# Optimization experiments

Hardware: AMD Instinct MI355X
Metric: run time of the kernel (lower is better)

## Reference

```python
import jax, jax.numpy as jnp
import numpy as np

B, C, H, W, D = 2, 256, 40, 40, 40
HEADS = 8


def _conv1x1(x, w, b):
    # 1x1x1 Conv3d == pointwise channel mix: x [B,C,H,W,D], w [O,C], b [O]
    return jnp.einsum('bchwd,oc->bohwd', x, w) + b[None, :, None, None, None]


def setup_inputs() -> dict:
    key = jax.random.key(0)
    ks = jax.random.split(key, 9)
    s = 1.0 / np.sqrt(C)
    return {
        'x': jax.random.normal(ks[0], (B, C, H, W, D), dtype=jnp.float32),
        'wq': jax.random.normal(ks[1], (C, C), dtype=jnp.float32) * s,
        'bq': jax.random.normal(ks[2], (C,), dtype=jnp.float32) * 0.01,
        'wk': jax.random.normal(ks[3], (C, C), dtype=jnp.float32) * s,
        'bk': jax.random.normal(ks[4], (C,), dtype=jnp.float32) * 0.01,
        'wv': jax.random.normal(ks[5], (C, C), dtype=jnp.float32) * s,
        'bv': jax.random.normal(ks[6], (C,), dtype=jnp.float32) * 0.01,
        'wp': jax.random.normal(ks[7], (C, C), dtype=jnp.float32) * s,
        'bp': jax.random.normal(ks[8], (C,), dtype=jnp.float32) * 0.01,
    }


def reference(x, wq, bq, wk, bk, wv, bv, wp, bp):
    b, ch, h, w, d = x.shape
    heads = HEADS
    hd = ch // heads
    scale = hd ** -0.5
    # q/k/v projections are identical across the three branches -> compute once
    q = _conv1x1(x, wq, bq)
    k = _conv1x1(x, wk, bk)
    v = _conv1x1(x, wv, bv)

    def branch(s1, s2, s3):
        # row-major reshape, exactly matching torch .view semantics
        qh = q.reshape(b, heads, hd, s1, s2, s3)
        kh = k.reshape(b, heads, hd, s1, s2, s3)
        vh = v.reshape(b, heads, hd, s1, s2, s3)
        # matmul over last two axes: attend along s2 with s3 as feature dim
        attn = jax.nn.softmax(qh @ jnp.swapaxes(kh, -1, -2) * scale, axis=-1)
        return (attn @ vh).reshape(b, ch, h, w, d)

    out = branch(h, w, d) + branch(w, h, d) + branch(d, h, w)
    return _conv1x1(out, wp, bp)
```

## Files before the change

### kernel.cpp

```cpp
#include <hip/hip_runtime.h>

#define NB 2
#define NC 256
#define NHH 40
#define NSP 64000
#define PL 1600
#define SCALE 0.17677669529663687f

typedef unsigned short u16;
typedef unsigned int   u32;

typedef __attribute__((ext_vector_type(8))) short bf16x8;
typedef __attribute__((ext_vector_type(4))) float f32x4;

__device__ __forceinline__ float bf2f(u16 u) {
    union { u32 i; float f; } c; c.i = ((u32)u) << 16; return c.f;
}
__device__ __forceinline__ u16 f2bf(float f) {
    union { u32 i; float f; } c; c.f = f; u32 x = c.i;
    return (u16)((x + 0x7fffu + ((x >> 16) & 1u)) >> 16);
}
__device__ __forceinline__ u32 pack2(float a, float b) {
    return (u32)f2bf(a) | ((u32)f2bf(b) << 16);
}
__device__ __forceinline__ f32x4 zero4() {
    f32x4 z; z[0] = 0.f; z[1] = 0.f; z[2] = 0.f; z[3] = 0.f; return z;
}
__device__ __forceinline__ bf16x8 zero8() {
    bf16x8 z;
#pragma unroll
    for (int e = 0; e < 8; ++e) z[e] = 0;
    return z;
}

__global__ __launch_bounds__(256) void wcvt3(
    const float* __restrict__ wq, const float* __restrict__ wk,
    const float* __restrict__ wv, u16* __restrict__ dst)
{
    const int g   = blockIdx.x * 256 + threadIdx.x;
    const int mat = g >> 14;
    const int off = (g & 16383) << 2;
    const float* s = (mat == 0) ? wq : ((mat == 1) ? wk : wv);
    const float4 f = *(const float4*)(s + off);
    ushort4 p;
    p.x = f2bf(f.x); p.y = f2bf(f.y); p.z = f2bf(f.z); p.w = f2bf(f.w);
    *(ushort4*)(dst + (mat << 16) + off) = p;
}

__global__ __launch_bounds__(256) void wcvt1(
    const float* __restrict__ w, u16* __restrict__ dst)
{
    const int g   = blockIdx.x * 256 + threadIdx.x;
    const int off = g << 2;
    const float4 f = *(const float4*)(w + off);
    ushort4 p;
    p.x = f2bf(f.x); p.y = f2bf(f.y); p.z = f2bf(f.z); p.w = f2bf(f.w);
    *(ushort4*)(dst + off) = p;
}

__global__ __launch_bounds__(256, 2) void qkv_mfma(
    const float* __restrict__ x, const u16* __restrict__ wb,
    const float* __restrict__ bq, const float* __restrict__ bk,
    const float* __restrict__ bv,
    u16* __restrict__ q, u16* __restrict__ k, u16* __restrict__ v)
{
    const int b    = blockIdx.z;
    const int n0   = blockIdx.x * 64;
    const int t    = threadIdx.x;
    const int lane = t & 63;
    const int wid  = t >> 6;
    const int o0w  = wid * 64;

    __shared__ u16 xs[64][264];
    __shared__ u16 wsm[2][256][40];

    const float* xb = x + (size_t)b * NC * NSP;

    {
        const int p   = t >> 4;
        const int nn  = (t & 15) << 2;
        const int rot = (t >> 1) & 3;
#pragma unroll
        for (int it = 0; it < 8; ++it) {
            const int c = (it * 16 + p) * 2;
            const float4 fa = *(const float4*)(xb + (size_t)c * NSP + n0 + nn);
            const float4 fb = *(const float4*)(xb + (size_t)(c + 1) * NSP + n0 + nn);
            u32 pk[4] = { pack2(fa.x, fb.x), pack2(fa.y, fb.y),
                          pack2(fa.z, fb.z), pack2(fa.w, fb.w) };
#pragma unroll
            for (int kk = 0; kk < 4; ++kk) {
                const int k2 = (kk + rot) & 3;
                *(u32*)&xs[nn + k2][c] = pk[k2];
            }
        }
    }

    {
        const u16* ws0 = wb + t * NC;
#pragma unroll
        for (int mm = 0; mm < 4; ++mm)
            *(bf16x8*)&wsm[0][t][mm * 8] = *(const bf16x8*)(ws0 + mm * 8);
    }
    __syncthreads();

    f32x4 acc[4][4];
#pragma unroll
    for (int i = 0; i < 4; ++i)
#pragma unroll
        for (int j = 0; j < 4; ++j) acc[i][j] = zero4();

    const int row = lane & 15;
    const int kg  = (lane >> 4) << 3;

    int cur = 0;
    for (int step = 0; step < 24; ++step) {
        const int m  = step >> 3;
        const int kc = step & 7;
        const bool pf = (step + 1 < 24);

        bf16x8 wreg[4];
        if (pf) {
            const int m2  = (step + 1) >> 3;
            const int kc2 = (step + 1) & 7;
            const u16* ws2 = wb + (m2 << 16) + t * NC + kc2 * 32;
#pragma unroll
            for (int mm = 0; mm < 4; ++mm)
                wreg[mm] = *(const bf16x8*)(ws2 + mm * 8);
        }

        bf16x8 af[4], bfr[4];
#pragma unroll
        for (int i = 0; i < 4; ++i)
            af[i] = *(const bf16x8*)&wsm[cur][o0w + 16 * i + row][kg];
#pragma unroll
        for (int j = 0; j < 4; ++j)
            bfr[j] = *(const bf16x8*)&xs[16 * j + row][kc * 32 + kg];
#pragma unroll
        for (int i = 0; i < 4; ++i)
#pragma unroll
            for (int j = 0; j < 4; ++j)
                acc[i][j] = __builtin_amdgcn_mfma_f32_16x16x32_bf16(
                    af[i], bfr[j], acc[i][j], 0, 0, 0);

        if (pf) {
#pragma unroll
            for (int mm = 0; mm < 4; ++mm)
                *(bf16x8*)&wsm[cur ^ 1][t][mm * 8] = wreg[mm];
        }

        if (kc == 7) {
            u16* op = ((m == 0) ? q : ((m == 1) ? k : v)) + (size_t)b * NC * NSP;
            const float* bm = (m == 0) ? bq : ((m == 1) ? bk : bv);
#pragma unroll
            for (int i = 0; i < 4; ++i) {
#pragma unroll
                for (int r = 0; r < 4; ++r) {
                    const int o = o0w + 16 * i + ((lane >> 4) << 2) + r;
                    const float bb = bm[o];
#pragma unroll
                    for (int j = 0; j < 4; ++j) {
                        const int n = n0 + 16 * j + row;
                        op[(size_t)o * NSP + n] = f2bf(acc[i][j][r] + bb);
                    }
                }
            }
#pragma unroll
            for (int i = 0; i < 4; ++i)
#pragma unroll
                for (int j = 0; j < 4; ++j) acc[i][j] = zero4();
        }

        if (pf) {
            __syncthreads();
            cur ^= 1;
        }
    }
}

__global__ __launch_bounds__(64, 4) void attn_mfma(
    const u16* __restrict__ q, const u16* __restrict__ k,
    const u16* __restrict__ v, u16* __restrict__ a)
{
    const int s = blockIdx.x;
    const size_t base = (size_t)s * PL;
    const int l = threadIdx.x & 63;
    const int g = l >> 4;
    const int c = l & 15;

    __shared__ u16 vs[48][56];
    __shared__ u16 ps[48][56];

#pragma unroll
    for (int it = 0; it < 3; ++it) {
        const int t = l + it * 64;
        *(u32*)&vs[t >> 2][40 + ((t & 3) << 1)] = 0u;
    }

#pragma unroll
    for (int it = 0; it < 7; ++it) {
        const int idx = l + it * 64;
        if (idx < 400) {
            const int j = idx / 10, d4 = (idx % 10) << 2;
            const ushort4 vv = *(const ushort4*)(v + base + j * 40 + d4);
            vs[d4 + 0][j] = vv.x; vs[d4 + 1][j] = vv.y;
            vs[d4 + 2][j] = vv.z; vs[d4 + 3][j] = vv.w;
        }
    }

    f32x4 sacc[3][3];
#pragma unroll
    for (int mt = 0; mt < 3; ++mt)
#pragma unroll
        for (int jt = 0; jt < 3; ++jt) sacc[mt][jt] = zero4();

    {
        bf16x8 aq[3], bk0[3];
#pragma unroll
        for (int mt = 0; mt < 3; ++mt)
            aq[mt] = *(const bf16x8*)(q + base + (size_t)(mt * 16 + c) * 40 + g * 8);
#pragma unroll
        for (int jt = 0; jt < 3; ++jt)
            bk0[jt] = *(const bf16x8*)(k + base + (size_t)(jt * 16 + c) * 40 + g * 8);
#pragma unroll
        for (int mt = 0; mt < 3; ++mt)
#pragma unroll
            for (int jt = 0; jt < 3; ++jt)
                sacc[mt][jt] = __builtin_amdgcn_mfma_f32_16x16x32_bf16(
                    aq[mt], bk0[jt], sacc[mt][jt], 0, 0, 0);

        bf16x8 aq1[3], bk1[3];
#pragma unroll
        for (int mt = 0; mt < 3; ++mt)
            aq1[mt] = (g == 0)
                ? *(const bf16x8*)(q + base + (size_t)(mt * 16 + c) * 40 + 32)
                : zero8();
#pragma unroll
        for (int jt = 0; jt < 3; ++jt)
            bk1[jt] = (g == 0)
                ? *(const bf16x8*)(k + base + (size_t)(jt * 16 + c) * 40 + 32)
                : zero8();
#pragma unroll
        for (int mt = 0; mt < 3; ++mt)
#pragma unroll
            for (int jt = 0; jt < 3; ++jt)
                sacc[mt][jt] = __builtin_amdgcn_mfma_f32_16x16x32_bf16(
                    aq1[mt], bk1[jt], sacc[mt][jt], 0, 0, 0);
    }

    const bool val2 = (c < 8);
#pragma unroll
    for (int mt = 0; mt < 3; ++mt) {
#pragma unroll
        for (int r = 0; r < 4; ++r) {
            const float v0 = sacc[mt][0][r];
            const float v1 = sacc[mt][1][r];
            const float v2 = sacc[mt][2][r];
            float mx = fmaxf(fmaxf(v0, v1), val2 ? v2 : -1e30f);
#pragma unroll
            for (int off = 1; off < 16; off <<= 1)
                mx = fmaxf(mx, __shfl_xor(mx, off, 64));
            const float p0 = __expf((v0 - mx) * SCALE);
            const float p1 = __expf((v1 - mx) * SCALE);
            const float p2 = val2 ? __expf((v2 - mx) * SCALE) : 0.f;
            float sum = p0 + p1 + p2;
#pragma unroll
            for (int off = 1; off < 16; off <<= 1)
                sum += __shfl_xor(sum, off, 64);
            const float inv = 3.0f / sum;
            const int ri = mt * 16 + g * 4 + r;
            ps[ri][c]      = f2bf(p0 * inv);
            ps[ri][c + 16] = f2bf(p1 * inv);
            ps[ri][c + 32] = f2bf(p2 * inv);
        }
    }
    __syncthreads();

    f32x4 oacc[3][3];
#pragma unroll
    for (int mt = 0; mt < 3; ++mt)
#pragma unroll
        for (int nt = 0; nt < 3; ++nt) oacc[mt][nt] = zero4();

    {
        bf16x8 pa[3], vb_[3];
#pragma unroll
        for (int mt = 0; mt < 3; ++mt)
            pa[mt] = *(const bf16x8*)&ps[mt * 16 + c][g * 8];
#pragma unroll
        for (int nt = 0; nt < 3; ++nt)
            vb_[nt] = *(const bf16x8*)&vs[nt * 16 + c][g * 8];
#pragma unroll
        for (int mt = 0; mt < 3; ++mt)
#pragma unroll
            for (int nt = 0; nt < 3; ++nt)
                oacc[mt][nt] = __builtin_amdgcn_mfma_f32_16x16x32_bf16(
                    pa[mt], vb_[nt], oacc[mt][nt], 0, 0, 0);

        bf16x8 pa1[3], vb1[3];
#pragma unroll
        for (int mt = 0; mt < 3; ++mt)
            pa1[mt] = (g < 2) ? *(const bf16x8*)&ps[mt * 16 + c][32 + g * 8] : zero8();
#pragma unroll
        for (int nt = 0; nt < 3; ++nt)
            vb1[nt] = (g < 2) ? *(const bf16x8*)&vs[nt * 16 + c][32 + g * 8] : zero8();
#pragma unroll
        for (int mt = 0; mt < 3; ++mt)
#pragma unroll
            for (int nt = 0; nt < 3; ++nt)
                oacc[mt][nt] = __builtin_amdgcn_mfma_f32_16x16x32_bf16(
                    pa1[mt], vb1[nt], oacc[mt][nt], 0, 0, 0);
    }
    __syncthreads();

#pragma unroll
    for (int mt = 0; mt < 3; ++mt) {
        if (mt == 2 && g >= 2) continue;
#pragma unroll
        for (int r = 0; r < 4; ++r) {
            const int ri = mt * 16 + g * 4 + r;
#pragma unroll
            for (int nt = 0; nt < 3; ++nt) {
                if (nt == 2 && c >= 8) continue;
                ps[ri][nt * 16 + c] = f2bf(oacc[mt][nt][r]);
            }
        }
    }
    __syncthreads();

#pragma unroll
    for (int it = 0; it < 7; ++it) {
        const int idx = l + it * 64;
        if (idx < 400) {
            const int i = idx / 10, d4 = (idx % 10) << 2;
            *(ushort4*)(a + base + (size_t)idx * 4) = *(const ushort4*)&ps[i][d4];
        }
    }
}

__global__ __launch_bounds__(256, 2) void proj_mfma(
    const u16* __restrict__ a, const u16* __restrict__ wpb,
    const float* __restrict__ bp, float* __restrict__ out)
{
    const int b    = blockIdx.z;
    const int n0   = blockIdx.x * 64;
    const int t    = threadIdx.x;
    const int lane = t & 63;
    const int wid  = t >> 6;
    const int o0w  = wid * 64;

    __shared__ u16 xs[64][264];
    __shared__ u16 wsm[2][256][40];

    const u16* ab = a + (size_t)b * NC * NSP;

    {
        const int p   = t >> 4;
        const int nn  = (t & 15) << 2;
        const int rot = (t >> 1) & 3;
#pragma unroll
        for (int it = 0; it < 8; ++it) {
            const int c = (it * 16 + p) * 2;
            const ushort4 ua = *(const ushort4*)(ab + (size_t)c * NSP + n0 + nn);
            const ushort4 ub = *(const ushort4*)(ab + (size_t)(c + 1) * NSP + n0 + nn);
            u32 pk[4] = { (u32)ua.x | ((u32)ub.x << 16), (u32)ua.y | ((u32)ub.y << 16),
                          (u32)ua.z | ((u32)ub.z << 16), (u32)ua.w | ((u32)ub.w << 16) };
#pragma unroll
            for (int kk = 0; kk < 4; ++kk) {
                const int k2 = (kk + rot) & 3;
                *(u32*)&xs[nn + k2][c] = pk[k2];
            }
        }
    }

    {
        const u16* ws0 = wpb + t * NC;
#pragma unroll
        for (int mm = 0; mm < 4; ++mm)
            *(bf16x8*)&wsm[0][t][mm * 8] = *(const bf16x8*)(ws0 + mm * 8);
    }
    __syncthreads();

    f32x4 acc[4][4];
#pragma unroll
    for (int i = 0; i < 4; ++i)
#pragma unroll
        for (int j = 0; j < 4; ++j) acc[i][j] = zero4();

    const int row = lane & 15;
    const int kg  = (lane >> 4) << 3;

    int cur = 0;
    for (int step = 0; step < 8; ++step) {
        const bool pf = (step + 1 < 8);
        bf16x8 wreg[4];
        if (pf) {
            const u16* ws2 = wpb + t * NC + (step + 1) * 32;
#pragma unroll
            for (int mm = 0; mm < 4; ++mm)
                wreg[mm] = *(const bf16x8*)(ws2 + mm * 8);
        }

        bf16x8 af[4], bfr[4];
#pragma unroll
        for (int i = 0; i < 4; ++i)
            af[i] = *(const bf16x8*)&wsm[cur][o0w + 16 * i + row][kg];
#pragma unroll
        for (int j = 0; j < 4; ++j)
            bfr[j] = *(const bf16x8*)&xs[16 * j + row][step * 32 + kg];
#pragma unroll
        for (int i = 0; i < 4; ++i)
#pragma unroll
            for (int j = 0; j < 4; ++j)
                acc[i][j] = __builtin_amdgcn_mfma_f32_16x16x32_bf16(
                    af[i], bfr[j], acc[i][j], 0, 0, 0);

        if (pf) {
#pragma unroll
            for (int mm = 0; mm < 4; ++mm)
                *(bf16x8*)&wsm[cur ^ 1][t][mm * 8] = wreg[mm];
            __syncthreads();
            cur ^= 1;
        }
    }

    float* ob = out + (size_t)b * NC * NSP;
#pragma unroll
    for (int i = 0; i < 4; ++i) {
#pragma unroll
        for (int r = 0; r < 4; ++r) {
            const int o = o0w + 16 * i + ((lane >> 4) << 2) + r;
            const float bb = bp[o];
#pragma unroll
            for (int j = 0; j < 4; ++j) {
                const int n = n0 + 16 * j + row;
                ob[(size_t)o * NSP + n] = acc[i][j][r] + bb;
            }
        }
    }
}

extern "C" void kernel_launch(void* const* d_in, const int* in_sizes, int n_in,
                              void* d_out, int out_size, void* d_ws, size_t ws_size,
                              hipStream_t stream)
{
    const float* x  = (const float*)d_in[0];
    const float* wq = (const float*)d_in[1];
    const float* bq = (const float*)d_in[2];
    const float* wk = (const float*)d_in[3];
    const float* bk = (const float*)d_in[4];
    const float* wv = (const float*)d_in[5];
    const float* bv = (const float*)d_in[6];
    const float* wp = (const float*)d_in[7];
    const float* bp = (const float*)d_in[8];
    float* out = (float*)d_out;

    const size_t QE = (size_t)NB * NC * NSP;
    u16* qb = (u16*)d_ws;
    u16* kb = qb + QE;
    u16* vb = kb + QE;
    u16* ab = vb + QE;

    u16* wqkv = (u16*)d_out;
    u16* wpb  = qb;

    wcvt3<<<192, 256, 0, stream>>>(wq, wk, wv, wqkv);
    qkv_mfma<<<dim3(NSP / 64, 1, NB), 256, 0, stream>>>(
        x, wqkv, bq, bk, bv, qb, kb, vb);
    attn_mfma<<<dim3(NB * NC * NHH), 64, 0, stream>>>(qb, kb, vb, ab);
    wcvt1<<<64, 256, 0, stream>>>(wp, wpb);
    proj_mfma<<<dim3(NSP / 64, 1, NB), 256, 0, stream>>>(ab, wpb, bp, out);
}
```

Before: 290.2 us.

## Read projection weights directly from global memory instead of double-buffered LDS

In the QKV and output projection kernels, the double-buffered shared-memory staging of the bf16 weight tiles is removed. MFMA A-fragments are now loaded straight from global memory, which is expected to hit in cache because the weights are small and shared by all blocks. This drops the per-step __syncthreads and frees about 40KB of LDS per block, and the launch bounds are raised to 4 blocks per CU to use the extra occupancy. The trade-off is more global/L2 traffic per MFMA step with no explicit prefetch, plus register pressure from the higher occupancy target.

```diff
diff --git a/kernel.cpp b/kernel.cpp
--- a/kernel.cpp
+++ b/kernel.cpp
@@ -58,7 +58,7 @@
     *(ushort4*)(dst + off) = p;
 }
 
-__global__ __launch_bounds__(256, 2) void qkv_mfma(
+__global__ __launch_bounds__(256, 4) void qkv_mfma(
     const float* __restrict__ x, const u16* __restrict__ wb,
     const float* __restrict__ bq, const float* __restrict__ bk,
     const float* __restrict__ bv,
@@ -72,7 +72,6 @@
     const int o0w  = wid * 64;
 
     __shared__ u16 xs[64][264];
-    __shared__ u16 wsm[2][256][40];
 
     const float* xb = x + (size_t)b * NC * NSP;
 
@@ -94,85 +93,52 @@
             }
         }
     }
-
-    {
-        const u16* ws0 = wb + t * NC;
-#pragma unroll
-        for (int mm = 0; mm < 4; ++mm)
-            *(bf16x8*)&wsm[0][t][mm * 8] = *(const bf16x8*)(ws0 + mm * 8);
-    }
     __syncthreads();
-
-    f32x4 acc[4][4];
-#pragma unroll
-    for (int i = 0; i < 4; ++i)
-#pragma unroll
-        for (int j = 0; j < 4; ++j) acc[i][j] = zero4();
 
     const int row = lane & 15;
     const int kg  = (lane >> 4) << 3;
 
-    int cur = 0;
-    for (int step = 0; step < 24; ++step) {
-        const int m  = step >> 3;
-        const int kc = step & 7;
-        const bool pf = (step + 1 < 24);
-
-        bf16x8 wreg[4];
-        if (pf) {
-            const int m2  = (step + 1) >> 3;
-            const int kc2 = (step + 1) & 7;
-            const u16* ws2 = wb + (m2 << 16) + t * NC + kc2 * 32;
-#pragma unroll
-            for (int mm = 0; mm < 4; ++mm)
-                wreg[mm] = *(const bf16x8*)(ws2 + mm * 8);
-        }
-
-        bf16x8 af[4], bfr[4];
+    for (int m = 0; m < 3; ++m) {
+        const u16* wm = wb + (m << 16);
+
+        f32x4 acc[4][4];
 #pragma unroll
         for (int i = 0; i < 4; ++i)
-            af[i] = *(const bf16x8*)&wsm[cur][o0w + 16 * i + row][kg];
-#pragma unroll
-        for (int j = 0; j < 4; ++j)
-            bfr[j] = *(const bf16x8*)&xs[16 * j + row][kc * 32 + kg];
-#pragma unroll
-        for (int i = 0; i < 4; ++i)
+#pragma unroll
+            for (int j = 0; j < 4; ++j) acc[i][j] = zero4();
+
+#pragma unroll
+        for (int kc = 0; kc < 8; ++kc) {
+            bf16x8 af[4], bfr[4];
+#pragma unroll
+            for (int i = 0; i < 4; ++i)
+                af[i] = *(const bf16x8*)(wm + (size_t)(o0w + 16 * i + row) * NC
+                                            + kc * 32 + kg);
 #pragma unroll
             for (int j = 0; j < 4; ++j)
-                acc[i][j] = __builtin_amdgcn_mfma_f32_16x16x32_bf16(
-                    af[i], bfr[j], acc[i][j], 0, 0, 0);
-
-        if (pf) {
-#pragma unroll
-            for (int mm = 0; mm < 4; ++mm)
-                *(bf16x8*)&wsm[cur ^ 1][t][mm * 8] = wreg[mm];
-        }
-
-        if (kc == 7) {
-            u16* op = ((m == 0) ? q : ((m == 1) ? k : v)) + (size_t)b * NC * NSP;
-            const float* bm = (m == 0) ? bq : ((m == 1) ? bk : bv);
-#pragma unroll
-            for (int i = 0; i < 4; ++i) {
-#pragma unroll
-                for (int r = 0; r < 4; ++r) {
-                    const int o = o0w + 16 * i + ((lane >> 4) << 2) + r;
-                    const float bb = bm[o];
-#pragma unroll
-                    for (int j = 0; j < 4; ++j) {
-                        const int n = n0 + 16 * j + row;
-                        op[(size_t)o * NSP + n] = f2bf(acc[i][j][r] + bb);
-                    }
+                bfr[j] = *(const bf16x8*)&xs[16 * j + row][kc * 32 + kg];
+#pragma unroll
+            for (int i = 0; i < 4; ++i)
+#pragma unroll
+                for (int j = 0; j < 4; ++j)
+                    acc[i][j] = __builtin_amdgcn_mfma_f32_16x16x32_bf16(
+                        af[i], bfr[j], acc[i][j], 0, 0, 0);
+        }
+
+        u16* op = ((m == 0) ? q : ((m == 1) ? k : v)) + (size_t)b * NC * NSP;
+        const float* bm = (m == 0) ? bq : ((m == 1) ? bk : bv);
+#pragma unroll
+        for (int i = 0; i < 4; ++i) {
+#pragma unroll
+            for (int r = 0; r < 4; ++r) {
+                const int o = o0w + 16 * i + ((lane >> 4) << 2) + r;
+                const float bb = bm[o];
+#pragma unroll
+                for (int j = 0; j < 4; ++j) {
+                    const int n = n0 + 16 * j + row;
+                    op[(size_t)o * NSP + n] = f2bf(acc[i][j][r] + bb);
                 }
             }
-#pragma unroll
-            for (int i = 0; i < 4; ++i)
-#pragma unroll
-                for (int j = 0; j < 4; ++j) acc[i][j] = zero4();
-        }
-
-        if (pf) {
-            __syncthreads();
-            cur ^= 1;
         }
     }
 }
@@ -337,7 +303,7 @@
     }
 }
 
-__global__ __launch_bounds__(256, 2) void proj_mfma(
+__global__ __launch_bounds__(256, 4) void proj_mfma(
     const u16* __restrict__ a, const u16* __restrict__ wpb,
     const float* __restrict__ bp, float* __restrict__ out)
 {
@@ -349,7 +315,6 @@
     const int o0w  = wid * 64;
 
     __shared__ u16 xs[64][264];
-    __shared__ u16 wsm[2][256][40];
 
     const u16* ab = a + (size_t)b * NC * NSP;
 
@@ -371,56 +336,33 @@
             }
         }
     }
-
-    {
-        const u16* ws0 = wpb + t * NC;
-#pragma unroll
-        for (int mm = 0; mm < 4; ++mm)
-            *(bf16x8*)&wsm[0][t][mm * 8] = *(const bf16x8*)(ws0 + mm * 8);
-    }
     __syncthreads();
-
-    f32x4 acc[4][4];
-#pragma unroll
-    for (int i = 0; i < 4; ++i)
-#pragma unroll
-        for (int j = 0; j < 4; ++j) acc[i][j] = zero4();
 
     const int row = lane & 15;
     const int kg  = (lane >> 4) << 3;
 
-    int cur = 0;
-    for (int step = 0; step < 8; ++step) {
-        const bool pf = (step + 1 < 8);
-        bf16x8 wreg[4];
-        if (pf) {
-            const u16* ws2 = wpb + t * NC + (step + 1) * 32;
-#pragma unroll
-            for (int mm = 0; mm < 4; ++mm)
-                wreg[mm] = *(const bf16x8*)(ws2 + mm * 8);
-        }
-
+    f32x4 acc[4][4];
+#pragma unroll
+    for (int i = 0; i < 4; ++i)
+#pragma unroll
+        for (int j = 0; j < 4; ++j) acc[i][j] = zero4();
+
+#pragma unroll
+    for (int kc = 0; kc < 8; ++kc) {
         bf16x8 af[4], bfr[4];
 #pragma unroll
         for (int i = 0; i < 4; ++i)
-            af[i] = *(const bf16x8*)&wsm[cur][o0w + 16 * i + row][kg];
+            af[i] = *(const bf16x8*)(wpb + (size_t)(o0w + 16 * i + row) * NC
+                                         + kc * 32 + kg);
 #pragma unroll
         for (int j = 0; j < 4; ++j)
-            bfr[j] = *(const bf16x8*)&xs[16 * j + row][step * 32 + kg];
+            bfr[j] = *(const bf16x8*)&xs[16 * j + row][kc * 32 + kg];
 #pragma unroll
         for (int i = 0; i < 4; ++i)
 #pragma unroll
             for (int j = 0; j < 4; ++j)
                 acc[i][j] = __builtin_amdgcn_mfma_f32_16x16x32_bf16(
                     af[i], bfr[j], acc[i][j], 0, 0, 0);
-
-        if (pf) {
-#pragma unroll
-            for (int mm = 0; mm < 4; ++mm)
-                *(bf16x8*)&wsm[cur ^ 1][t][mm * 8] = wreg[mm];
-            __syncthreads();
-            cur ^= 1;
-        }
     }
 
     float* ob = out + (size_t)b * NC * NSP;
```

After: 506.9 us. +74.7%, slower.
